# Performance work log

Hardware: AMD Instinct MI355X
Metric: run time of the kernel (lower is better)

Reference implementation:

```python
import jax, jax.numpy as jnp
import numpy as np

S, B, D, H, WIN, L = 8192, 4, 512, 8, 64, 6
HD = D // H
EPS = 1e-5


def setup_inputs() -> dict:
    key = jax.random.key(0)
    ks = jax.random.split(key, 6)
    s = 0.02
    return {
        "src": jax.random.normal(ks[0], (S, B, D), jnp.float32),
        "Wqkv": jax.random.normal(ks[1], (L, 3 * D, D), jnp.float32) * s,
        "bqkv": jnp.zeros((L, 3 * D), jnp.float32),
        "Wo": jax.random.normal(ks[2], (L, D, D), jnp.float32) * s,
        "bo": jnp.zeros((L, D), jnp.float32),
        "W1": jax.random.normal(ks[3], (L, 4 * D, D), jnp.float32) * s,
        "bf1": jnp.zeros((L, 4 * D), jnp.float32),
        "W2": jax.random.normal(ks[4], (L, D, 4 * D), jnp.float32) * s,
        "bf2": jnp.zeros((L, D), jnp.float32),
        "g1": jnp.ones((L, D), jnp.float32),
        "beta1": jnp.zeros((L, D), jnp.float32),
        "g2": jnp.ones((L, D), jnp.float32),
        "beta2": jnp.zeros((L, D), jnp.float32),
    }


def layernorm(x, g, b):
    m = jnp.mean(x, axis=-1, keepdims=True)
    v = jnp.mean(jnp.square(x - m), axis=-1, keepdims=True)
    return (x - m) * jax.lax.rsqrt(v + EPS) * g + b


def _forward(src, Wqkv, bqkv, Wo, bo, W1, bf1, W2, bf2, g1, beta1, g2, beta2):
    NW = S // WIN
    scale = 1.0 / np.sqrt(HD)
    x = src
    for l in range(L):
        qkv = x @ Wqkv[l].T + bqkv[l]                      # (S,B,3D)
        q, k, v = jnp.split(qkv, 3, axis=-1)
        win = lambda t: t.reshape(NW, WIN, B, H, HD)       # (NW,W,B,H,hd)
        q = win(q) * scale
        k = win(k)
        v = win(v)
        att = jax.nn.softmax(jnp.einsum('nqbhd,nkbhd->nbhqk', q, k), axis=-1)
        o = jnp.einsum('nbhqk,nkbhd->nqbhd', att, v).reshape(S, B, D)
        o = o @ Wo[l].T + bo[l]
        x = layernorm(x + o, g1[l], beta1[l])
        # FFN with ReLU (hidden = 4*d_model)
        f = jax.nn.relu(x @ W1[l].T + bf1[l]) @ W2[l].T + bf2[l]
        x = layernorm(x + f, g2[l], beta2[l])
    return x


def reference(src, Wqkv, bqkv, Wo, bo, W1, bf1, W2, bf2, g1, beta1, g2, beta2):
    return _forward(src, Wqkv, bqkv, Wo, bo, W1, bf1, W2, bf2, g1, beta1, g2, beta2)
```

## Files before the change

### kernel.cpp

```cpp
#include <hip/hip_runtime.h>
#include <hip/hip_bf16.h>

typedef __bf16 bf16x8 __attribute__((ext_vector_type(8)));
typedef float f32x4 __attribute__((ext_vector_type(4)));

static constexpr int NT = 32768;
static constexpr int D_ = 512;
static constexpr int D3 = 1536;
static constexpr int DF = 2048;
static constexpr int L_ = 6;

#define AS1 __attribute__((address_space(1)))
#define AS3 __attribute__((address_space(3)))

__device__ __forceinline__ void gload_lds16(const void* g, void* l) {
  __builtin_amdgcn_global_load_lds((const AS1 void*)g, (AS3 void*)l, 16, 0, 0);
}

template<int K, int NTN, bool RELU>
__global__ __launch_bounds__(256, 2) void gemm128(
    const __hip_bfloat16* __restrict__ A,
    const __hip_bfloat16* __restrict__ W,
    const float* __restrict__ bias,
    __hip_bfloat16* __restrict__ Cout) {
  __shared__ __align__(16) char lds[65536];
  const int t = threadIdx.x;
  const int l = t & 63, w = t >> 6;
  const int lrow = l & 15, lhi = l >> 4;
  const int wr = w >> 1, wc = w & 1;

  const int lin = blockIdx.x;
  const int wg = (lin & 7) * ((int)gridDim.x >> 3) + (lin >> 3);
  const int tm0 = (wg / NTN) * 128, tn0 = (wg % NTN) * 128;

  constexpr int NKT = K / 64;
  constexpr int NIT = NKT / 2;
  constexpr int N = NTN * 128;

  const int srow = t >> 3;
  const int sun = t & 7;

  const int u8 = (sun ^ (srow & 7)) << 3;
  const __hip_bfloat16* sA = A + (size_t)(tm0 + srow) * K + u8;
  const __hip_bfloat16* sA2 = sA + (size_t)64 * K;
  const __hip_bfloat16* sW = W + (size_t)(tn0 + srow) * K + u8;
  const __hip_bfloat16* sW2 = sW + (size_t)64 * K;

  const int lo = lrow * 128;
  const int x0 = (lhi ^ (lrow & 7)) << 4;
  const int x1 = ((4 + lhi) ^ (lrow & 7)) << 4;
  const char* pA[2][2];
  const char* pB[2][2];
  pA[0][0] = lds + (0 * 4 + wr) * 8192 + lo + x0;
  pA[0][1] = lds + (0 * 4 + wr) * 8192 + lo + x1;
  pA[1][0] = lds + (1 * 4 + wr) * 8192 + lo + x0;
  pA[1][1] = lds + (1 * 4 + wr) * 8192 + lo + x1;
  pB[0][0] = lds + (0 * 4 + 2 + wc) * 8192 + lo + x0;
  pB[0][1] = lds + (0 * 4 + 2 + wc) * 8192 + lo + x1;
  pB[1][0] = lds + (1 * 4 + 2 + wc) * 8192 + lo + x0;
  pB[1][1] = lds + (1 * 4 + 2 + wc) * 8192 + lo + x1;

  auto stage = [&](int buf, int reg, const __hip_bfloat16* s, int kt) {
    char* dst = lds + (buf * 4 + reg) * 8192 + w * 1024;
    const __hip_bfloat16* src = s + kt * 64;
    gload_lds16(src, dst);
    gload_lds16(src + (size_t)32 * K, dst + 4096);
  };

  f32x4 acc[4][4] = {};
  bf16x8 bfrag[4][2], afrag[2][2];

  stage(0, 2, sW, 0);
  stage(0, 3, sW2, 0);
  stage(0, 0, sA, 0);
  stage(0, 1, sA2, 0);
  stage(1, 2, sW, 1);
  stage(1, 3, sW2, 1);
  asm volatile("s_waitcnt vmcnt(4)" ::: "memory");
  __builtin_amdgcn_sched_barrier(0);
  __builtin_amdgcn_s_barrier();

#define MPHASE(BUF, RB, MB0, MB1, STG, VMS)                                 \
  {                                                                          \
    if (RB) {                                                                \
      _Pragma("unroll") for (int n = 0; n < 4; ++n)                          \
          _Pragma("unroll") for (int ks = 0; ks < 2; ++ks)                   \
              bfrag[n][ks] = *(const bf16x8*)(pB[BUF][ks] + n * 2048);       \
    }                                                                        \
    _Pragma("unroll") for (int ks = 0; ks < 2; ++ks) {                       \
      afrag[0][ks] = *(const bf16x8*)(pA[BUF][ks] + MB0 * 2048);             \
      afrag[1][ks] = *(const bf16x8*)(pA[BUF][ks] + MB1 * 2048);             \
    }                                                                        \
    STG;                                                                     \
    _Pragma("unroll") for (int n = 0; n < 4; ++n)                            \
        _Pragma("unroll") for (int ks = 0; ks < 2; ++ks) {                   \
      acc[MB0][n] = __builtin_amdgcn_mfma_f32_16x16x32_bf16(                 \
          afrag[0][ks], bfrag[n][ks], acc[MB0][n], 0, 0, 0);                 \
      acc[MB1][n] = __builtin_amdgcn_mfma_f32_16x16x32_bf16(                 \
          afrag[1][ks], bfrag[n][ks], acc[MB1][n], 0, 0, 0);                 \
    }                                                                        \
    VMS;                                                                     \
    asm volatile("s_waitcnt lgkmcnt(0)" ::: "memory");                       \
    __builtin_amdgcn_sched_barrier(0);                                       \
    __builtin_amdgcn_s_barrier();                                            \
  }

#define VM_CNT                                              \
  if (more) {                                               \
    asm volatile("s_waitcnt vmcnt(4)" ::: "memory");        \
  } else {                                                  \
    asm volatile("s_waitcnt vmcnt(0)" ::: "memory");        \
  }

  for (int it = 0; it < NIT; ++it) {
    const int t1 = 2 * it + 1;
    const bool more = (it + 1 < NIT);
    MPHASE(0, 1, 0, 1, { stage(1, 0, sA, t1); stage(1, 1, sA2, t1); }, );
    MPHASE(0, 0, 2, 3,
           { if (more) { stage(0, 2, sW, t1 + 1); stage(0, 3, sW2, t1 + 1); } },
           VM_CNT);
    MPHASE(1, 1, 0, 1,
           { if (more) { stage(0, 0, sA, t1 + 1); stage(0, 1, sA2, t1 + 1); } }, );
    MPHASE(1, 0, 2, 3,
           { if (more) { stage(1, 2, sW, t1 + 2); stage(1, 3, sW2, t1 + 2); } },
           VM_CNT);
  }
#undef MPHASE
#undef VM_CNT

  char* ep = lds + w * 8192;
#pragma unroll
  for (int n = 0; n < 4; ++n) {
    float bv = bias[tn0 + wc * 64 + n * 16 + lrow];
#pragma unroll
    for (int m = 0; m < 4; ++m)
#pragma unroll
      for (int j = 0; j < 4; ++j) {
        float v = acc[m][n][j] + bv;
        if (RELU) v = fmaxf(v, 0.f);
        int row = m * 16 + lhi * 4 + j;
        int col = n * 16 + lrow;
        *(__hip_bfloat16*)(ep + row * 128 + (((col >> 3) ^ (row & 7)) << 4) +
                           (col & 7) * 2) = __float2bfloat16(v);
      }
  }
  __builtin_amdgcn_sched_barrier(0);
  const int er = l >> 3, ec = l & 7;
#pragma unroll
  for (int p = 0; p < 8; ++p) {
    int r = p * 8 + er;
    uint4 vv = *(const uint4*)(ep + r * 128 + ((ec ^ (r & 7)) << 4));
    *(uint4*)&Cout[(size_t)(tm0 + wr * 64 + r) * N + tn0 + wc * 64 + ec * 8] = vv;
  }
}

__global__ __launch_bounds__(128) void attn_win(
    const __hip_bfloat16* __restrict__ qkv, __hip_bfloat16* __restrict__ o) {
  __shared__ __align__(16) char lds[2 * 18432];
  const int t = threadIdx.x, l = t & 63, w = t >> 6;
  char* vt = lds + w * 18432;
  char* pl = vt + 9216;
  const int wid = blockIdx.x * 2 + w;
  const int h = wid & 7, b = (wid >> 3) & 3, nw = wid >> 5;
  const int lrow = l & 15, lhi = l >> 4;
  const __hip_bfloat16* qp = qkv + (size_t)(nw * 256 + b) * 1536 + h * 64;
  const __hip_bfloat16* kp = qp + 512;
  const __hip_bfloat16* vp = qp + 1024;

  {
    const int d0 = (l & 7) * 8;
    const int r0 = l >> 3;
#pragma unroll
    for (int i = 0; i < 8; ++i) {
      int r = r0 + i * 8;
      union { uint4 u; __hip_bfloat16 e[8]; } vv;
      vv.u = *(const uint4*)(vp + (size_t)r * 6144 + d0);
#pragma unroll
      for (int j = 0; j < 8; ++j)
        *(__hip_bfloat16*)(vt + ((d0 + j) * 72 + r) * 2) = vv.e[j];
    }
  }

  bf16x8 qf[4][2], kf[4][2];
#pragma unroll
  for (int mi = 0; mi < 4; ++mi)
#pragma unroll
    for (int ks = 0; ks < 2; ++ks) {
      int r = mi * 16 + lrow;
      int d = ks * 32 + lhi * 8;
      qf[mi][ks] = __builtin_bit_cast(bf16x8, *(const uint4*)(qp + (size_t)r * 6144 + d));
      kf[mi][ks] = __builtin_bit_cast(bf16x8, *(const uint4*)(kp + (size_t)r * 6144 + d));
    }

  f32x4 s[4][4] = {};
#pragma unroll
  for (int mi = 0; mi < 4; ++mi)
#pragma unroll
    for (int ni = 0; ni < 4; ++ni) {
      s[mi][ni] = __builtin_amdgcn_mfma_f32_16x16x32_bf16(qf[mi][0], kf[ni][0], s[mi][ni], 0, 0, 0);
      s[mi][ni] = __builtin_amdgcn_mfma_f32_16x16x32_bf16(qf[mi][1], kf[ni][1], s[mi][ni], 0, 0, 0);
    }

#pragma unroll
  for (int mi = 0; mi < 4; ++mi)
#pragma unroll
    for (int j = 0; j < 4; ++j) {
      float mx = s[mi][0][j];
#pragma unroll
      for (int ni = 1; ni < 4; ++ni) mx = fmaxf(mx, s[mi][ni][j]);
      mx = fmaxf(mx, __shfl_xor(mx, 1));
      mx = fmaxf(mx, __shfl_xor(mx, 2));
      mx = fmaxf(mx, __shfl_xor(mx, 4));
      mx = fmaxf(mx, __shfl_xor(mx, 8));
      float p[4], sum = 0.f;
#pragma unroll
      for (int ni = 0; ni < 4; ++ni) { p[ni] = __expf(s[mi][ni][j] - mx); sum += p[ni]; }
      sum += __shfl_xor(sum, 1);
      sum += __shfl_xor(sum, 2);
      sum += __shfl_xor(sum, 4);
      sum += __shfl_xor(sum, 8);
      float inv = 1.f / sum;
      int row = mi * 16 + lhi * 4 + j;
#pragma unroll
      for (int ni = 0; ni < 4; ++ni)
        *(__hip_bfloat16*)(pl + (row * 72 + ni * 16 + lrow) * 2) =
            __float2bfloat16(p[ni] * inv);
    }

  bf16x8 pf[4][2], vf[4][2];
#pragma unroll
  for (int mi = 0; mi < 4; ++mi)
#pragma unroll
    for (int ks = 0; ks < 2; ++ks)
      pf[mi][ks] = *(const bf16x8*)(pl + ((mi * 16 + lrow) * 72 + ks * 32 + lhi * 8) * 2);
#pragma unroll
  for (int ni = 0; ni < 4; ++ni)
#pragma unroll
    for (int ks = 0; ks < 2; ++ks)
      vf[ni][ks] = *(const bf16x8*)(vt + ((ni * 16 + lrow) * 72 + ks * 32 + lhi * 8) * 2);

  f32x4 acc[4][4] = {};
#pragma unroll
  for (int mi = 0; mi < 4; ++mi)
#pragma unroll
    for (int ni = 0; ni < 4; ++ni) {
      acc[mi][ni] = __builtin_amdgcn_mfma_f32_16x16x32_bf16(pf[mi][0], vf[ni][0], acc[mi][ni], 0, 0, 0);
      acc[mi][ni] = __builtin_amdgcn_mfma_f32_16x16x32_bf16(pf[mi][1], vf[ni][1], acc[mi][ni], 0, 0, 0);
    }

  __hip_bfloat16* op = o + (size_t)(nw * 256 + b) * 512 + h * 64;
#pragma unroll
  for (int mi = 0; mi < 4; ++mi)
#pragma unroll
    for (int ni = 0; ni < 4; ++ni) {
      int col = ni * 16 + lrow;
#pragma unroll
      for (int j = 0; j < 4; ++j) {
        int row = mi * 16 + lhi * 4 + j;
        op[(size_t)row * 2048 + col] = __float2bfloat16(acc[mi][ni][j]);
      }
    }
}

template<bool LAST>
__global__ __launch_bounds__(256) void ln_res_b(
    __hip_bfloat16* __restrict__ xb, const __hip_bfloat16* __restrict__ f,
    const float* __restrict__ g, const float* __restrict__ be,
    float* __restrict__ xout) {
  const int w = threadIdx.x >> 6, l = threadIdx.x & 63;
  const size_t row = (size_t)blockIdx.x * 4 + w;
  const int c = l * 8;
  union { uint4 u; __hip_bfloat16 e[8]; } xa, fa;
  xa.u = *(const uint4*)(xb + row * 512 + c);
  fa.u = *(const uint4*)(f + row * 512 + c);
  float v[8];
#pragma unroll
  for (int j = 0; j < 8; ++j)
    v[j] = __bfloat162float(xa.e[j]) + __bfloat162float(fa.e[j]);
  float sum = 0.f, sq = 0.f;
#pragma unroll
  for (int j = 0; j < 8; ++j) { sum += v[j]; sq += v[j] * v[j]; }
#pragma unroll
  for (int m = 1; m < 64; m <<= 1) {
    sum += __shfl_xor(sum, m);
    sq += __shfl_xor(sq, m);
  }
  float mean = sum * (1.f / 512.f);
  float var = sq * (1.f / 512.f) - mean * mean;
  float rs = rsqrtf(var + 1e-5f);
  float4 g0 = *(const float4*)(g + c);
  float4 g1v = *(const float4*)(g + c + 4);
  float4 e0 = *(const float4*)(be + c);
  float4 e1 = *(const float4*)(be + c + 4);
  float gg[8] = {g0.x, g0.y, g0.z, g0.w, g1v.x, g1v.y, g1v.z, g1v.w};
  float ee[8] = {e0.x, e0.y, e0.z, e0.w, e1.x, e1.y, e1.z, e1.w};
  float y[8];
  union { uint4 u; __hip_bfloat16 e[8]; } hb;
#pragma unroll
  for (int j = 0; j < 8; ++j) {
    y[j] = (v[j] - mean) * rs * gg[j] + ee[j];
    hb.e[j] = __float2bfloat16(y[j]);
  }
  *(uint4*)(xb + row * 512 + c) = hb.u;
  if (LAST) {
    float4 o0 = {y[0], y[1], y[2], y[3]};
    float4 o1 = {y[4], y[5], y[6], y[7]};
    *(float4*)(xout + row * 512 + c) = o0;
    *(float4*)(xout + row * 512 + c + 4) = o1;
  }
}

__global__ void convq(const float* __restrict__ wq, __hip_bfloat16* __restrict__ o) {
  int i = blockIdx.x * 256 + threadIdx.x;
  float4 v = ((const float4*)wq)[i];
  int e = i * 4;
  float sc = (((e >> 9) % 1536) < 512) ? 0.125f : 1.f;
  __hip_bfloat16 hb[4] = {__float2bfloat16(v.x * sc), __float2bfloat16(v.y * sc),
                          __float2bfloat16(v.z * sc), __float2bfloat16(v.w * sc)};
  ((uint2*)o)[i] = *(uint2*)hb;
}

__global__ void convw(const float* __restrict__ s, __hip_bfloat16* __restrict__ o) {
  int i = blockIdx.x * 256 + threadIdx.x;
  float4 v = ((const float4*)s)[i];
  __hip_bfloat16 hb[4] = {__float2bfloat16(v.x), __float2bfloat16(v.y),
                          __float2bfloat16(v.z), __float2bfloat16(v.w)};
  ((uint2*)o)[i] = *(uint2*)hb;
}

__global__ void scaleb(const float* __restrict__ b, float* __restrict__ o) {
  int i = blockIdx.x * 256 + threadIdx.x;
  o[i] = b[i] * (((i % 1536) < 512) ? 0.125f : 1.f);
}

extern "C" void kernel_launch(void* const* d_in, const int* in_sizes, int n_in,
                              void* d_out, int out_size, void* d_ws, size_t ws_size,
                              hipStream_t stream) {
  const float* src  = (const float*)d_in[0];
  const float* Wqkv = (const float*)d_in[1];
  const float* bqkv = (const float*)d_in[2];
  const float* Wo   = (const float*)d_in[3];
  const float* bo   = (const float*)d_in[4];
  const float* W1   = (const float*)d_in[5];
  const float* bf1  = (const float*)d_in[6];
  const float* W2   = (const float*)d_in[7];
  const float* bf2  = (const float*)d_in[8];
  const float* g1   = (const float*)d_in[9];
  const float* be1  = (const float*)d_in[10];
  const float* g2   = (const float*)d_in[11];
  const float* be2  = (const float*)d_in[12];
  float* xout = (float*)d_out;

  char* ws = (char*)d_ws;
  size_t off = 0;
  auto alloc = [&](size_t bytes) {
    char* p = ws + off;
    off += (bytes + 255) & ~(size_t)255;
    return p;
  };

  const size_t wq_b = (size_t)L_ * D3 * D_ * 2;
  const size_t wo_b = (size_t)L_ * D_ * D_ * 2;
  const size_t w1_b = (size_t)L_ * DF * D_ * 2;
  const size_t w2_b = (size_t)L_ * D_ * DF * 2;
  const size_t xb_b = (size_t)NT * 512 * 2;
  auto al = [](size_t v) { return (v + 255) & ~(size_t)255; };
  const size_t persist =
      al(wq_b) + al(wo_b) + al(w1_b) + al(w2_b) + al(L_ * D3 * 4) + al(xb_b);

  int CT = NT;
  while (CT > 2048 && persist + (size_t)CT * 5120 + 65536 > ws_size) CT >>= 1;

  __hip_bfloat16* wqkvb = (__hip_bfloat16*)alloc(wq_b);
  __hip_bfloat16* wob   = (__hip_bfloat16*)alloc(wo_b);
  __hip_bfloat16* w1b   = (__hip_bfloat16*)alloc(w1_b);
  __hip_bfloat16* w2b   = (__hip_bfloat16*)alloc(w2_b);
  float*          bqs   = (float*)alloc((size_t)L_ * D3 * 4);
  __hip_bfloat16* xb    = (__hip_bfloat16*)alloc(xb_b);
  __hip_bfloat16* R     = (__hip_bfloat16*)alloc((size_t)CT * 2048 * 2);
  __hip_bfloat16* OB    = (__hip_bfloat16*)alloc((size_t)CT * 512 * 2);

  convw<<<NT * 512 / 4 / 256, 256, 0, stream>>>(src, xb);
  convq<<<L_ * D3 * D_ / 4 / 256, 256, 0, stream>>>(Wqkv, wqkvb);
  convw<<<L_ * D_ * D_ / 4 / 256, 256, 0, stream>>>(Wo, wob);
  convw<<<L_ * DF * D_ / 4 / 256, 256, 0, stream>>>(W1, w1b);
  convw<<<L_ * D_ * DF / 4 / 256, 256, 0, stream>>>(W2, w2b);
  scaleb<<<L_ * D3 / 256, 256, 0, stream>>>(bqkv, bqs);

  const int nch = NT / CT;
  for (int c = 0; c < nch; ++c) {
    __hip_bfloat16* xm = xb + (size_t)c * CT * 512;
    float* xo = xout + (size_t)c * CT * 512;
    for (int l = 0; l < L_; ++l) {
      gemm128<512, 12, false><<<(CT / 128) * 12, 256, 0, stream>>>(
          xm, wqkvb + (size_t)l * D3 * D_, bqs + l * D3, R);
      attn_win<<<CT / 16, 128, 0, stream>>>(R, OB);
      gemm128<512, 4, false><<<(CT / 128) * 4, 256, 0, stream>>>(
          OB, wob + (size_t)l * D_ * D_, bo + l * D_, R);
      ln_res_b<false><<<CT / 4, 256, 0, stream>>>(xm, R, g1 + l * D_,
                                                  be1 + l * D_, xo);
      gemm128<512, 16, true><<<(CT / 128) * 16, 256, 0, stream>>>(
          xm, w1b + (size_t)l * DF * D_, bf1 + l * DF, R);
      gemm128<2048, 4, false><<<(CT / 128) * 4, 256, 0, stream>>>(
          R, w2b + (size_t)l * D_ * DF, bf2 + l * D_, OB);
      if (l == L_ - 1)
        ln_res_b<true><<<CT / 4, 256, 0, stream>>>(xm, OB, g2 + l * D_,
                                                   be2 + l * D_, xo);
      else
        ln_res_b<false><<<CT / 4, 256, 0, stream>>>(xm, OB, g2 + l * D_,
                                                    be2 + l * D_, xo);
    }
  }
}
```

Baseline: 1.850 ms.

## Prepack weights into MFMA fragment layout and load B directly to registers

```diff
diff --git a/kernel.cpp b/kernel.cpp
--- a/kernel.cpp
+++ b/kernel.cpp
@@ -18,12 +18,12 @@
 }
 
 template<int K, int NTN, bool RELU>
-__global__ __launch_bounds__(256, 2) void gemm128(
+__global__ __launch_bounds__(256, 3) void gemm128g(
     const __hip_bfloat16* __restrict__ A,
-    const __hip_bfloat16* __restrict__ W,
+    const __hip_bfloat16* __restrict__ Wp,
     const float* __restrict__ bias,
     __hip_bfloat16* __restrict__ Cout) {
-  __shared__ __align__(16) char lds[65536];
+  __shared__ __align__(16) char lds[32768];
   const int t = threadIdx.x;
   const int l = t & 63, w = t >> 6;
   const int lrow = l & 15, lhi = l >> 4;
@@ -34,99 +34,95 @@
   const int tm0 = (wg / NTN) * 128, tn0 = (wg % NTN) * 128;
 
   constexpr int NKT = K / 64;
-  constexpr int NIT = NKT / 2;
   constexpr int N = NTN * 128;
 
   const int srow = t >> 3;
   const int sun = t & 7;
-
   const int u8 = (sun ^ (srow & 7)) << 3;
   const __hip_bfloat16* sA = A + (size_t)(tm0 + srow) * K + u8;
   const __hip_bfloat16* sA2 = sA + (size_t)64 * K;
-  const __hip_bfloat16* sW = W + (size_t)(tn0 + srow) * K + u8;
-  const __hip_bfloat16* sW2 = sW + (size_t)64 * K;
+
+  const char* bpB = (const char*)(Wp + (size_t)((tn0 >> 6) + wc) * NKT * 4096) +
+                    l * 16;
 
   const int lo = lrow * 128;
   const int x0 = (lhi ^ (lrow & 7)) << 4;
   const int x1 = ((4 + lhi) ^ (lrow & 7)) << 4;
   const char* pA[2][2];
-  const char* pB[2][2];
-  pA[0][0] = lds + (0 * 4 + wr) * 8192 + lo + x0;
-  pA[0][1] = lds + (0 * 4 + wr) * 8192 + lo + x1;
-  pA[1][0] = lds + (1 * 4 + wr) * 8192 + lo + x0;
-  pA[1][1] = lds + (1 * 4 + wr) * 8192 + lo + x1;
-  pB[0][0] = lds + (0 * 4 + 2 + wc) * 8192 + lo + x0;
-  pB[0][1] = lds + (0 * 4 + 2 + wc) * 8192 + lo + x1;
-  pB[1][0] = lds + (1 * 4 + 2 + wc) * 8192 + lo + x0;
-  pB[1][1] = lds + (1 * 4 + 2 + wc) * 8192 + lo + x1;
-
-  auto stage = [&](int buf, int reg, const __hip_bfloat16* s, int kt) {
-    char* dst = lds + (buf * 4 + reg) * 8192 + w * 1024;
-    const __hip_bfloat16* src = s + kt * 64;
-    gload_lds16(src, dst);
-    gload_lds16(src + (size_t)32 * K, dst + 4096);
+  pA[0][0] = lds + wr * 8192 + lo + x0;
+  pA[0][1] = lds + wr * 8192 + lo + x1;
+  pA[1][0] = lds + 16384 + wr * 8192 + lo + x0;
+  pA[1][1] = lds + 16384 + wr * 8192 + lo + x1;
+
+  auto stageA = [&](int p, int kt) {
+    char* d0 = lds + p * 16384 + w * 1024;
+    const __hip_bfloat16* s0 = sA + kt * 64;
+    gload_lds16(s0, d0);
+    gload_lds16(s0 + (size_t)32 * K, d0 + 4096);
+    char* d1 = lds + p * 16384 + 8192 + w * 1024;
+    const __hip_bfloat16* s1 = sA2 + kt * 64;
+    gload_lds16(s1, d1);
+    gload_lds16(s1 + (size_t)32 * K, d1 + 4096);
   };
+  auto loadB = [&](bf16x8 (&bf)[4][2], int kt) {
+    const char* q = bpB + (size_t)kt * 8192;
+#pragma unroll
+    for (int n = 0; n < 4; ++n)
+#pragma unroll
+      for (int ks = 0; ks < 2; ++ks)
+        bf[n][ks] = *(const bf16x8*)(q + (n * 2 + ks) * 1024);
+  };
 
   f32x4 acc[4][4] = {};
-  bf16x8 bfrag[4][2], afrag[2][2];
-
-  stage(0, 2, sW, 0);
-  stage(0, 3, sW2, 0);
-  stage(0, 0, sA, 0);
-  stage(0, 1, sA2, 0);
-  stage(1, 2, sW, 1);
-  stage(1, 3, sW2, 1);
-  asm volatile("s_waitcnt vmcnt(4)" ::: "memory");
+  bf16x8 bfA[4][2], bfB[4][2], af[2][2];
+
+  stageA(0, 0);
+  __builtin_amdgcn_sched_barrier(0);
+  loadB(bfA, 0);
+  asm volatile("s_waitcnt vmcnt(8)" ::: "memory");
   __builtin_amdgcn_sched_barrier(0);
   __builtin_amdgcn_s_barrier();
 
-#define MPHASE(BUF, RB, MB0, MB1, STG, VMS)                                 \
+#define SUB(P, BF, MB)                                                      \
   {                                                                          \
-    if (RB) {                                                                \
-      _Pragma("unroll") for (int n = 0; n < 4; ++n)                          \
-          _Pragma("unroll") for (int ks = 0; ks < 2; ++ks)                   \
-              bfrag[n][ks] = *(const bf16x8*)(pB[BUF][ks] + n * 2048);       \
+    _Pragma("unroll") for (int ks = 0; ks < 2; ++ks) {                       \
+      af[0][ks] = *(const bf16x8*)(pA[P][ks] + (MB) * 2048);                 \
+      af[1][ks] = *(const bf16x8*)(pA[P][ks] + (MB + 1) * 2048);             \
     }                                                                        \
-    _Pragma("unroll") for (int ks = 0; ks < 2; ++ks) {                       \
-      afrag[0][ks] = *(const bf16x8*)(pA[BUF][ks] + MB0 * 2048);             \
-      afrag[1][ks] = *(const bf16x8*)(pA[BUF][ks] + MB1 * 2048);             \
-    }                                                                        \
-    STG;                                                                     \
     _Pragma("unroll") for (int n = 0; n < 4; ++n)                            \
         _Pragma("unroll") for (int ks = 0; ks < 2; ++ks) {                   \
-      acc[MB0][n] = __builtin_amdgcn_mfma_f32_16x16x32_bf16(                 \
-          afrag[0][ks], bfrag[n][ks], acc[MB0][n], 0, 0, 0);                 \
-      acc[MB1][n] = __builtin_amdgcn_mfma_f32_16x16x32_bf16(                 \
-          afrag[1][ks], bfrag[n][ks], acc[MB1][n], 0, 0, 0);                 \
+      acc[MB][n] = __builtin_amdgcn_mfma_f32_16x16x32_bf16(                  \
+          af[0][ks], BF[n][ks], acc[MB][n], 0, 0, 0);                        \
+      acc[MB + 1][n] = __builtin_amdgcn_mfma_f32_16x16x32_bf16(              \
+          af[1][ks], BF[n][ks], acc[MB + 1][n], 0, 0, 0);                    \
     }                                                                        \
-    VMS;                                                                     \
-    asm volatile("s_waitcnt lgkmcnt(0)" ::: "memory");                       \
-    __builtin_amdgcn_sched_barrier(0);                                       \
-    __builtin_amdgcn_s_barrier();                                            \
-  }
-
-#define VM_CNT                                              \
-  if (more) {                                               \
-    asm volatile("s_waitcnt vmcnt(4)" ::: "memory");        \
-  } else {                                                  \
-    asm volatile("s_waitcnt vmcnt(0)" ::: "memory");        \
-  }
-
-  for (int it = 0; it < NIT; ++it) {
-    const int t1 = 2 * it + 1;
-    const bool more = (it + 1 < NIT);
-    MPHASE(0, 1, 0, 1, { stage(1, 0, sA, t1); stage(1, 1, sA2, t1); }, );
-    MPHASE(0, 0, 2, 3,
-           { if (more) { stage(0, 2, sW, t1 + 1); stage(0, 3, sW2, t1 + 1); } },
-           VM_CNT);
-    MPHASE(1, 1, 0, 1,
-           { if (more) { stage(0, 0, sA, t1 + 1); stage(0, 1, sA2, t1 + 1); } }, );
-    MPHASE(1, 0, 2, 3,
-           { if (more) { stage(1, 2, sW, t1 + 2); stage(1, 3, sW2, t1 + 2); } },
-           VM_CNT);
-  }
-#undef MPHASE
-#undef VM_CNT
+  }
+#define CLOSE(VM)                                                           \
+  if (VM) asm volatile("s_waitcnt vmcnt(8)" ::: "memory");                  \
+  asm volatile("s_waitcnt lgkmcnt(0)" ::: "memory");                        \
+  __builtin_amdgcn_sched_barrier(0);                                        \
+  __builtin_amdgcn_s_barrier();
+
+  for (int it = 0; it < NKT / 2; ++it) {
+    const int k1 = 2 * it + 1;
+    const bool more = (it + 1 < NKT / 2);
+    stageA(1, k1);
+    __builtin_amdgcn_sched_barrier(0);
+    loadB(bfB, k1);
+    SUB(0, bfA, 0)
+    SUB(0, bfA, 2)
+    CLOSE(1)
+    if (more) {
+      stageA(0, k1 + 1);
+      __builtin_amdgcn_sched_barrier(0);
+      loadB(bfA, k1 + 1);
+    }
+    SUB(1, bfB, 0)
+    SUB(1, bfB, 2)
+    CLOSE(more)
+  }
+#undef SUB
+#undef CLOSE
 
   char* ep = lds + w * 8192;
 #pragma unroll
@@ -310,22 +306,29 @@
   }
 }
 
-__global__ void convq(const float* __restrict__ wq, __hip_bfloat16* __restrict__ o) {
-  int i = blockIdx.x * 256 + threadIdx.x;
-  float4 v = ((const float4*)wq)[i];
-  int e = i * 4;
-  float sc = (((e >> 9) % 1536) < 512) ? 0.125f : 1.f;
-  __hip_bfloat16 hb[4] = {__float2bfloat16(v.x * sc), __float2bfloat16(v.y * sc),
-                          __float2bfloat16(v.z * sc), __float2bfloat16(v.w * sc)};
-  ((uint2*)o)[i] = *(uint2*)hb;
-}
-
 __global__ void convw(const float* __restrict__ s, __hip_bfloat16* __restrict__ o) {
   int i = blockIdx.x * 256 + threadIdx.x;
   float4 v = ((const float4*)s)[i];
   __hip_bfloat16 hb[4] = {__float2bfloat16(v.x), __float2bfloat16(v.y),
                           __float2bfloat16(v.z), __float2bfloat16(v.w)};
   ((uint2*)o)[i] = *(uint2*)hb;
+}
+
+template<int K, int Nw, bool SCALEQ>
+__global__ void convs(const float* __restrict__ s, __hip_bfloat16* __restrict__ o) {
+  int i = blockIdx.x * 256 + threadIdx.x;
+  int e = i * 4;
+  int layer = e / (Nw * K);
+  int rem = e - layer * (Nw * K);
+  int r = rem / K, c = rem - r * K;
+  float4 v = ((const float4*)s)[i];
+  float sc = (SCALEQ && r < 512) ? 0.125f : 1.f;
+  int didx = layer * (Nw * K) + ((r >> 6) * (K >> 6) + (c >> 6)) * 4096 +
+             (((r >> 4) & 3) * 2 + ((c >> 5) & 1)) * 512 + ((c >> 3) & 3) * 128 +
+             (r & 15) * 8 + (c & 7);
+  __hip_bfloat16 hb[4] = {__float2bfloat16(v.x * sc), __float2bfloat16(v.y * sc),
+                          __float2bfloat16(v.z * sc), __float2bfloat16(v.w * sc)};
+  *(uint2*)(o + didx) = *(uint2*)hb;
 }
 
 __global__ void scaleb(const float* __restrict__ b, float* __restrict__ o) {
@@ -381,10 +384,10 @@
   __hip_bfloat16* OB    = (__hip_bfloat16*)alloc((size_t)CT * 512 * 2);
 
   convw<<<NT * 512 / 4 / 256, 256, 0, stream>>>(src, xb);
-  convq<<<L_ * D3 * D_ / 4 / 256, 256, 0, stream>>>(Wqkv, wqkvb);
-  convw<<<L_ * D_ * D_ / 4 / 256, 256, 0, stream>>>(Wo, wob);
-  convw<<<L_ * DF * D_ / 4 / 256, 256, 0, stream>>>(W1, w1b);
-  convw<<<L_ * D_ * DF / 4 / 256, 256, 0, stream>>>(W2, w2b);
+  convs<512, 1536, true><<<L_ * D3 * D_ / 4 / 256, 256, 0, stream>>>(Wqkv, wqkvb);
+  convs<512, 512, false><<<L_ * D_ * D_ / 4 / 256, 256, 0, stream>>>(Wo, wob);
+  convs<512, 2048, false><<<L_ * DF * D_ / 4 / 256, 256, 0, stream>>>(W1, w1b);
+  convs<2048, 512, false><<<L_ * D_ * DF / 4 / 256, 256, 0, stream>>>(W2, w2b);
   scaleb<<<L_ * D3 / 256, 256, 0, stream>>>(bqkv, bqs);
 
   const int nch = NT / CT;
@@ -392,16 +395,16 @@
     __hip_bfloat16* xm = xb + (size_t)c * CT * 512;
     float* xo = xout + (size_t)c * CT * 512;
     for (int l = 0; l < L_; ++l) {
-      gemm128<512, 12, false><<<(CT / 128) * 12, 256, 0, stream>>>(
+      gemm128g<512, 12, false><<<(CT / 128) * 12, 256, 0, stream>>>(
           xm, wqkvb + (size_t)l * D3 * D_, bqs + l * D3, R);
       attn_win<<<CT / 16, 128, 0, stream>>>(R, OB);
-      gemm128<512, 4, false><<<(CT / 128) * 4, 256, 0, stream>>>(
+      gemm128g<512, 4, false><<<(CT / 128) * 4, 256, 0, stream>>>(
           OB, wob + (size_t)l * D_ * D_, bo + l * D_, R);
       ln_res_b<false><<<CT / 4, 256, 0, stream>>>(xm, R, g1 + l * D_,
                                                   be1 + l * D_, xo);
-      gemm128<512, 16, true><<<(CT / 128) * 16, 256, 0, stream>>>(
+      gemm128g<512, 16, true><<<(CT / 128) * 16, 256, 0, stream>>>(
           xm, w1b + (size_t)l * DF * D_, bf1 + l * DF, R);
-      gemm128<2048, 4, false><<<(CT / 128) * 4, 256, 0, stream>>>(
+      gemm128g<2048, 4, false><<<(CT / 128) * 4, 256, 0, stream>>>(
           R, w2b + (size_t)l * D_ * DF, bf2 + l * D_, OB);
       if (l == L_ - 1)
         ln_res_b<true><<<CT / 4, 256, 0, stream>>>(xm, OB, g2 + l * D_,
```

Result: no change. 1.816 ms (-1.9%).
